# Performance work log

Measured on AMD Instinct MI355X. Metric: run time of the kernel, lower is better.

Reference implementation:

```python
import jax, jax.numpy as jnp
import numpy as np


def setup_inputs() -> dict:
    key = jax.random.key(0)
    k1, k2, k3 = jax.random.split(key, 3)
    B, N, D = 512, 128, 3
    pred = jax.random.normal(k1, (B, N, D), dtype=jnp.float32)
    gt = jax.random.normal(k2, (B, N, D), dtype=jnp.float32)
    weights = jax.random.uniform(k3, (B,), dtype=jnp.float32)
    sigma = jnp.ones((), dtype=jnp.float32)  # init sigma = 1.0 (learnable param)
    return {"pred": pred, "gt": gt, "weights": weights, "sigma": sigma}


def reference(pred, gt, weights, sigma):
    # pred, gt: [B, N, D]
    noise_var = sigma ** 2
    # pairwise: norms[i, j] = mean_n ||gt[j, n] - pred[i, n]||_2
    diff = gt[None, :, :, :] - pred[:, None, :, :]          # [B, B, N, D]
    norms = jnp.sqrt(jnp.sum(diff * diff, axis=-1)).mean(-1)  # [B, B]
    logits = -0.5 * (norms ** 2) / noise_var                 # [B, B]
    # cross entropy vs identity targets, reduction='none'
    log_probs = jax.nn.log_softmax(logits, axis=-1)
    loss = -jnp.diagonal(log_probs)                          # [B]
    loss = loss * jax.lax.stop_gradient(2.0 * noise_var)
    loss = loss * weights
    return loss
```

## Files before the change

kernel.cpp:

```cpp
#include <hip/hip_runtime.h>

#define B 512
#define N 128
#define NG (N / 4)
#define TI 2

__device__ __forceinline__ float dist4(const float4 a0, const float4 a1, const float4 a2,
                                       const float4 b0, const float4 b1, const float4 b2) {
    float dx, dy, dz, s, r;
    dx = a0.x - b0.x; dy = a0.y - b0.y; dz = a0.z - b0.z;
    s = dx * dx + dy * dy + dz * dz; r = sqrtf(s);
    dx = a0.w - b0.w; dy = a1.x - b1.x; dz = a1.y - b1.y;
    s = dx * dx + dy * dy + dz * dz; r += sqrtf(s);
    dx = a1.z - b1.z; dy = a1.w - b1.w; dz = a2.x - b2.x;
    s = dx * dx + dy * dy + dz * dz; r += sqrtf(s);
    dx = a2.y - b2.y; dy = a2.z - b2.z; dz = a2.w - b2.w;
    s = dx * dx + dy * dy + dz * dz; r += sqrtf(s);
    return r;
}

__global__ __launch_bounds__(512) void vmse_kernel(const float* __restrict__ pred,
                                                   const float* __restrict__ gt,
                                                   const float* __restrict__ w,
                                                   const float* __restrict__ sigma,
                                                   float* __restrict__ out) {
    __shared__ __align__(16) float spred[TI * N * 3];
    __shared__ float lbuf[TI][B];
    __shared__ float wred[2][TI][8];

    const int t = threadIdx.x;
    const int i0 = blockIdx.x * TI;

    {
        const float4* psrc = (const float4*)(pred + (size_t)i0 * (N * 3));
        float4* pdst = (float4*)spred;
        if (t < (TI * N * 3) / 4) pdst[t] = psrc[t];
    }
    __syncthreads();

    const float nv = sigma[0] * sigma[0];

    const int j = t;
    const float4* grow = (const float4*)(gt + (size_t)j * (N * 3));
    const float4* prow0 = (const float4*)(spred);
    const float4* prow1 = (const float4*)(spred + N * 3);

    float acc0 = 0.f, acc1 = 0.f;
#pragma unroll 2
    for (int g = 0; g < NG; ++g) {
        const float4 g0 = grow[3 * g + 0];
        const float4 g1 = grow[3 * g + 1];
        const float4 g2 = grow[3 * g + 2];
        const float4 p00 = prow0[3 * g + 0];
        const float4 p01 = prow0[3 * g + 1];
        const float4 p02 = prow0[3 * g + 2];
        const float4 p10 = prow1[3 * g + 0];
        const float4 p11 = prow1[3 * g + 1];
        const float4 p12 = prow1[3 * g + 2];
        acc0 += dist4(g0, g1, g2, p00, p01, p02);
        acc1 += dist4(g0, g1, g2, p10, p11, p12);
    }

    const float norm0 = acc0 * (1.f / N);
    const float norm1 = acc1 * (1.f / N);
    float l0 = -0.5f * norm0 * norm0 / nv;
    float l1 = -0.5f * norm1 * norm1 / nv;
    lbuf[0][j] = l0;
    lbuf[1][j] = l1;

    float m0 = l0, m1 = l1;
    for (int off = 32; off; off >>= 1) {
        m0 = fmaxf(m0, __shfl_xor(m0, off));
        m1 = fmaxf(m1, __shfl_xor(m1, off));
    }
    const int wid = t >> 6, lane = t & 63;
    if (lane == 0) { wred[0][0][wid] = m0; wred[0][1][wid] = m1; }
    __syncthreads();

    float rm0 = -1e30f, rm1 = -1e30f;
#pragma unroll
    for (int k = 0; k < 8; ++k) {
        rm0 = fmaxf(rm0, wred[0][0][k]);
        rm1 = fmaxf(rm1, wred[0][1][k]);
    }

    float e0 = __expf(l0 - rm0), e1 = __expf(l1 - rm1);
    for (int off = 32; off; off >>= 1) {
        e0 += __shfl_xor(e0, off);
        e1 += __shfl_xor(e1, off);
    }
    if (lane == 0) { wred[1][0][wid] = e0; wred[1][1][wid] = e1; }
    __syncthreads();

    if (t == 0) {
        float s0 = 0.f, s1 = 0.f;
#pragma unroll
        for (int k = 0; k < 8; ++k) { s0 += wred[1][0][k]; s1 += wred[1][1][k]; }
        const float lse0 = rm0 + __logf(s0);
        const float lse1 = rm1 + __logf(s1);
        const float d0 = lbuf[0][i0];
        const float d1 = lbuf[1][i0 + 1];
        out[i0]     = (lse0 - d0) * 2.f * nv * w[i0];
        out[i0 + 1] = (lse1 - d1) * 2.f * nv * w[i0 + 1];
    }
}

extern "C" void kernel_launch(void* const* d_in, const int* in_sizes, int n_in,
                              void* d_out, int out_size, void* d_ws, size_t ws_size,
                              hipStream_t stream) {
    const float* pred  = (const float*)d_in[0];
    const float* gt    = (const float*)d_in[1];
    const float* wts   = (const float*)d_in[2];
    const float* sigma = (const float*)d_in[3];
    float* out = (float*)d_out;

    hipLaunchKernelGGL(vmse_kernel, dim3(B / TI), dim3(512), 0, stream,
                       pred, gt, wts, sigma, out);
}
```

Baseline: 89.32 us.

## Transpose gt into workspace for coalesced loads; read pred directly from global

Adds a pre-pass kernel that transposes gt into a float4-interleaved layout in workspace, so that each thread's gt loads in the main loop are coalesced across the wavefront rather than strided by 1536 bytes per row. The main kernel drops the shared-memory staging of pred and reads it directly as uniform global loads, and keeps only the two diagonal logits in shared memory instead of the full logits buffer. The unroll factor rises to 4. In exchange it costs an extra kernel launch and a round trip of gt through workspace memory.

```diff
diff --git a/kernel.cpp b/kernel.cpp
--- a/kernel.cpp
+++ b/kernel.cpp
@@ -2,7 +2,7 @@
 
 #define B 512
 #define N 128
-#define NG (N / 4)
+#define NQ 96
 #define TI 2
 
 __device__ __forceinline__ float dist4(const float4 a0, const float4 a1, const float4 a2,
@@ -19,54 +19,53 @@
     return r;
 }
 
-__global__ __launch_bounds__(512) void vmse_kernel(const float* __restrict__ pred,
-                                                   const float* __restrict__ gt,
-                                                   const float* __restrict__ w,
-                                                   const float* __restrict__ sigma,
-                                                   float* __restrict__ out) {
-    __shared__ __align__(16) float spred[TI * N * 3];
-    __shared__ float lbuf[TI][B];
+__global__ __launch_bounds__(256) void transpose_gt(const float4* __restrict__ gt4,
+                                                    float4* __restrict__ gtT) {
+    const int tid = blockIdx.x * 256 + threadIdx.x;
+    const int j = tid / NQ;
+    const int q = tid - j * NQ;
+    gtT[q * B + j] = gt4[tid];
+}
+
+__global__ __launch_bounds__(512) void vmse_main(const float* __restrict__ pred,
+                                                 const float4* __restrict__ gtT,
+                                                 const float* __restrict__ w,
+                                                 const float* __restrict__ sigma,
+                                                 float* __restrict__ out) {
+    __shared__ float sdiag[TI];
     __shared__ float wred[2][TI][8];
 
     const int t = threadIdx.x;
     const int i0 = blockIdx.x * TI;
 
-    {
-        const float4* psrc = (const float4*)(pred + (size_t)i0 * (N * 3));
-        float4* pdst = (float4*)spred;
-        if (t < (TI * N * 3) / 4) pdst[t] = psrc[t];
+    const float4* p0 = (const float4*)(pred + (size_t)i0 * (N * 3));
+    const float4* p1 = p0 + NQ;
+
+    float acc0 = 0.f, acc1 = 0.f;
+#pragma unroll 4
+    for (int g = 0; g < 32; ++g) {
+        const float4 g0 = gtT[(3 * g + 0) * B + t];
+        const float4 g1 = gtT[(3 * g + 1) * B + t];
+        const float4 g2 = gtT[(3 * g + 2) * B + t];
+        const float4 a0 = p0[3 * g + 0];
+        const float4 a1 = p0[3 * g + 1];
+        const float4 a2 = p0[3 * g + 2];
+        const float4 b0 = p1[3 * g + 0];
+        const float4 b1 = p1[3 * g + 1];
+        const float4 b2 = p1[3 * g + 2];
+        acc0 += dist4(g0, g1, g2, a0, a1, a2);
+        acc1 += dist4(g0, g1, g2, b0, b1, b2);
     }
-    __syncthreads();
 
     const float nv = sigma[0] * sigma[0];
+    const float c = -0.5f / nv;
+    const float n0 = acc0 * (1.f / N);
+    const float n1 = acc1 * (1.f / N);
+    const float l0 = n0 * n0 * c;
+    const float l1 = n1 * n1 * c;
 
-    const int j = t;
-    const float4* grow = (const float4*)(gt + (size_t)j * (N * 3));
-    const float4* prow0 = (const float4*)(spred);
-    const float4* prow1 = (const float4*)(spred + N * 3);
-
-    float acc0 = 0.f, acc1 = 0.f;
-#pragma unroll 2
-    for (int g = 0; g < NG; ++g) {
-        const float4 g0 = grow[3 * g + 0];
-        const float4 g1 = grow[3 * g + 1];
-        const float4 g2 = grow[3 * g + 2];
-        const float4 p00 = prow0[3 * g + 0];
-        const float4 p01 = prow0[3 * g + 1];
-        const float4 p02 = prow0[3 * g + 2];
-        const float4 p10 = prow1[3 * g + 0];
-        const float4 p11 = prow1[3 * g + 1];
-        const float4 p12 = prow1[3 * g + 2];
-        acc0 += dist4(g0, g1, g2, p00, p01, p02);
-        acc1 += dist4(g0, g1, g2, p10, p11, p12);
-    }
-
-    const float norm0 = acc0 * (1.f / N);
-    const float norm1 = acc1 * (1.f / N);
-    float l0 = -0.5f * norm0 * norm0 / nv;
-    float l1 = -0.5f * norm1 * norm1 / nv;
-    lbuf[0][j] = l0;
-    lbuf[1][j] = l1;
+    if (t == i0)     sdiag[0] = l0;
+    if (t == i0 + 1) sdiag[1] = l1;
 
     float m0 = l0, m1 = l1;
     for (int off = 32; off; off >>= 1) {
@@ -98,10 +97,8 @@
         for (int k = 0; k < 8; ++k) { s0 += wred[1][0][k]; s1 += wred[1][1][k]; }
         const float lse0 = rm0 + __logf(s0);
         const float lse1 = rm1 + __logf(s1);
-        const float d0 = lbuf[0][i0];
-        const float d1 = lbuf[1][i0 + 1];
-        out[i0]     = (lse0 - d0) * 2.f * nv * w[i0];
-        out[i0 + 1] = (lse1 - d1) * 2.f * nv * w[i0 + 1];
+        out[i0]     = (lse0 - sdiag[0]) * 2.f * nv * w[i0];
+        out[i0 + 1] = (lse1 - sdiag[1]) * 2.f * nv * w[i0 + 1];
     }
 }
 
@@ -113,7 +110,10 @@
     const float* wts   = (const float*)d_in[2];
     const float* sigma = (const float*)d_in[3];
     float* out = (float*)d_out;
+    float4* gtT = (float4*)d_ws;
 
-    hipLaunchKernelGGL(vmse_kernel, dim3(B / TI), dim3(512), 0, stream,
-                       pred, gt, wts, sigma, out);
+    hipLaunchKernelGGL(transpose_gt, dim3((B * NQ) / 256), dim3(256), 0, stream,
+                       (const float4*)gt, gtT);
+    hipLaunchKernelGGL(vmse_main, dim3(B / TI), dim3(512), 0, stream,
+                       pred, gtT, wts, sigma, out);
 }
```

After: 86.90 us. 1.03x faster.
